# Performance work log

Measured on AMD Instinct MI355X. Metric: run time of the kernel, lower is better.

The kernel has to match this reference:

```python
import jax, jax.numpy as jnp
import numpy as np

N_EXPERTS = 64
TOPK = 4
DIM = 2048
B_T = 8192


def setup_inputs() -> dict:
    key = jax.random.key(0)
    k1, k2 = jax.random.split(key)
    x = jax.random.normal(k1, (B_T, DIM), jnp.float32)
    W = jax.random.normal(k2, (N_EXPERTS, DIM), jnp.float32) * 0.02  # nn.Linear weight (out, in)
    router_bias = jnp.zeros((N_EXPERTS,), jnp.float32)  # registered buffer, init zeros
    return {"x": x, "W": W, "router_bias": router_bias, "token_capacity": 3072}


def _route(x, W, router_bias, token_capacity):
    """Faithful serial greedy capacity-aware routing.

    Replicates the torch nested loop (k-major, token-minor order):
      - per step, pick argmax over the token's (mutated) logits among experts
        with remaining capacity;
      - full experts whose logit exceeds the chosen one get permanently set
        to -inf in that token's logit row (exactly what the inner while-style
        loop does);
      - if no expert has capacity, selected stays -1, weight 0, and the whole
        row becomes -inf (torch sets the top expert to -inf n_experts times).
    """
    logits0 = x @ W.T + router_bias                       # (N, E)
    scores = jax.nn.softmax(logits0, axis=-1)             # (N, E)
    cap = token_capacity // TOPK                          # python int
    remaining0 = jnp.full((N_EXPERTS,), float(cap), jnp.float32)
    N = x.shape[0]
    NEG = jnp.float32(-jnp.inf)

    def step(carry, i):
        logits, remaining = carry
        b = i % N                                         # token index (k-major order)
        row = logits[b]                                   # (E,)
        masked = jnp.where(remaining > 0, row, NEG)
        chosen = jnp.argmax(masked)
        ok = remaining[chosen] > 0                        # False only if all experts full
        sel = jnp.where(ok, chosen, -1).astype(jnp.int32)
        w = jnp.where(ok, scores[b, chosen], jnp.float32(0.0))
        full = remaining <= 0
        cval = row[chosen]
        # full experts 'above' the chosen one were visited and zapped to -inf
        new_row = jnp.where(ok,
                            jnp.where(full & (row > cval), NEG, row),
                            jnp.full_like(row, NEG))
        logits = logits.at[b].set(new_row)
        remaining = remaining.at[chosen].add(jnp.where(ok, jnp.float32(-1.0), jnp.float32(0.0)))
        return (logits, remaining), (sel, w)

    (_, _), (sel_f, w_f) = jax.lax.scan(step, (logits0, remaining0),
                                        jnp.arange(TOPK * N))
    selected = sel_f.reshape(TOPK, N).T                   # (N, TOPK)
    weights = w_f.reshape(TOPK, N).T                      # (N, TOPK)
    weights = weights / (weights.sum(axis=-1, keepdims=True) + 1e-8)
    return selected, weights


def reference(x, W, router_bias, token_capacity):
    return _route(x, W, router_bias, token_capacity)
```

## Files before the change

### kernel.cpp

```cpp
#include <hip/hip_runtime.h>
#include <math.h>

#define N_TOK 8192
#define DIM   2048
#define NE    64
#define TOPK  4
#define THETA 2e-3f
#define TPB   32
#define NBLK  (N_TOK / TPB)
#define HSTR  16

typedef short bf16x8 __attribute__((ext_vector_type(8)));
typedef float f32x4  __attribute__((ext_vector_type(4)));

#define OFF_LOGITS 0
#define OFF_MAXV   (OFF_LOGITS + N_TOK * NE)
#define OFF_DENOM  (OFF_MAXV + N_TOK)
#define OFF_HIST   (OFF_DENOM + N_TOK)
#define OFF_WT     (OFF_HIST + NE * HSTR)
#define OFF_WTMP   (OFF_WT + NE * DIM)

__device__ inline void cvt2(float a, float b, unsigned& hi, unsigned& lo) {
    const unsigned ua = __float_as_uint(a), ub = __float_as_uint(b);
    hi = __builtin_amdgcn_perm(ub, ua, 0x07060302u);
    const float ra = a - __uint_as_float(ua & 0xFFFF0000u);
    const float rb = b - __uint_as_float(ub & 0xFFFF0000u);
    lo = __builtin_amdgcn_perm(__float_as_uint(rb), __float_as_uint(ra), 0x07060302u);
}

union FragU { unsigned u[4]; bf16x8 v; uint4 q; };

__device__ inline void make_frags(const float4& p, const float4& q,
                                  bf16x8& hi, bf16x8& lo) {
    FragU H, L;
    cvt2(p.x, p.y, H.u[0], L.u[0]);
    cvt2(p.z, p.w, H.u[1], L.u[1]);
    cvt2(q.x, q.y, H.u[2], L.u[2]);
    cvt2(q.z, q.w, H.u[3], L.u[3]);
    hi = H.v; lo = L.v;
}

__global__ __launch_bounds__(256)
void k_wc(const float* __restrict__ W, float* __restrict__ wt,
          int* __restrict__ hist) {
    const int t = blockIdx.x * 256 + threadIdx.x;
    if (t < NE * HSTR) hist[t] = 0;
    const int l  = t & 63;
    const int grp = t >> 6;
    const int nt = grp & 3;
    const int kc = grp >> 2;
    const int e  = nt * 16 + (l & 15);
    const int k0 = kc * 32 + (l >> 4) * 8;

    const float4 p = *reinterpret_cast<const float4*>(W + (size_t)e * DIM + k0);
    const float4 q = *reinterpret_cast<const float4*>(W + (size_t)e * DIM + k0 + 4);
    wt[(size_t)(k0 + 0) * NE + e] = p.x;
    wt[(size_t)(k0 + 1) * NE + e] = p.y;
    wt[(size_t)(k0 + 2) * NE + e] = p.z;
    wt[(size_t)(k0 + 3) * NE + e] = p.w;
    wt[(size_t)(k0 + 4) * NE + e] = q.x;
    wt[(size_t)(k0 + 5) * NE + e] = q.y;
    wt[(size_t)(k0 + 6) * NE + e] = q.z;
    wt[(size_t)(k0 + 7) * NE + e] = q.w;
}

__global__ __launch_bounds__(512, 2)
void k_main(const float* __restrict__ x, const float* __restrict__ W,
            const float* __restrict__ bias, const float* __restrict__ wt,
            float* __restrict__ logits, float* __restrict__ maxv,
            float* __restrict__ denomv, int* __restrict__ hist,
            float* __restrict__ out) {
    __shared__ float red[8][TPB][68];
    __shared__ float lbuf[TPB][68];
    __shared__ int   selS[TPB];
    __shared__ float wS[TPB];
    __shared__ short flagIdx[TPB];
    __shared__ int   flagCnt;

    const int tid = threadIdx.x;
    const int w   = tid >> 6;
    const int l   = tid & 63;
    const int t0  = blockIdx.x * TPB;
    const int m   = l & 15;
    const int g   = l >> 4;

    if (tid == 0) flagCnt = 0;

    const float* aP0 = x + (size_t)(t0 + m) * DIM + w * 32 + g * 8;
    const float* aP1 = aP0 + (size_t)16 * DIM;
    const float* bP  = W + (size_t)m * DIM + w * 32 + g * 8;

    f32x4 accA[2][4], accB[2][4];
    #pragma unroll
    for (int t = 0; t < 2; ++t)
        #pragma unroll
        for (int nt = 0; nt < 4; ++nt)
            #pragma unroll
            for (int r = 0; r < 4; ++r) { accA[t][nt][r] = 0.0f; accB[t][nt][r] = 0.0f; }

    float4 cA[2][4], cB[2][8];
    cA[0][0] = *reinterpret_cast<const float4*>(aP0);
    cA[0][1] = *reinterpret_cast<const float4*>(aP0 + 4);
    cA[0][2] = *reinterpret_cast<const float4*>(aP1);
    cA[0][3] = *reinterpret_cast<const float4*>(aP1 + 4);
    #pragma unroll
    for (int nt = 0; nt < 4; ++nt) {
        cB[0][nt * 2 + 0] = *reinterpret_cast<const float4*>(bP + (size_t)nt * 16 * DIM);
        cB[0][nt * 2 + 1] = *reinterpret_cast<const float4*>(bP + (size_t)nt * 16 * DIM + 4);
    }

    #pragma unroll
    for (int win = 0; win < 8; ++win) {
        const int cur = win & 1, nxt = cur ^ 1;
        if (win < 7) {
            const int ko = (win + 1) * 256;
            cA[nxt][0] = *reinterpret_cast<const float4*>(aP0 + ko);
            cA[nxt][1] = *reinterpret_cast<const float4*>(aP0 + ko + 4);
            cA[nxt][2] = *reinterpret_cast<const float4*>(aP1 + ko);
            cA[nxt][3] = *reinterpret_cast<const float4*>(aP1 + ko + 4);
            #pragma unroll
            for (int nt = 0; nt < 4; ++nt) {
                cB[nxt][nt * 2 + 0] =
                    *reinterpret_cast<const float4*>(bP + (size_t)nt * 16 * DIM + ko);
                cB[nxt][nt * 2 + 1] =
                    *reinterpret_cast<const float4*>(bP + (size_t)nt * 16 * DIM + ko + 4);
            }
        }

        bf16x8 bh[4], bl[4];
        #pragma unroll
        for (int nt = 0; nt < 4; ++nt)
            make_frags(cB[cur][nt * 2], cB[cur][nt * 2 + 1], bh[nt], bl[nt]);

        #pragma unroll
        for (int t = 0; t < 2; ++t) {
            bf16x8 ah, al;
            make_frags(cA[cur][t * 2], cA[cur][t * 2 + 1], ah, al);
            #pragma unroll
            for (int nt = 0; nt < 4; ++nt) {
                accA[t][nt] = __builtin_amdgcn_mfma_f32_16x16x32_bf16(ah, bh[nt], accA[t][nt], 0, 0, 0);
                accB[t][nt] = __builtin_amdgcn_mfma_f32_16x16x32_bf16(al, bh[nt], accB[t][nt], 0, 0, 0);
            }
            #pragma unroll
            for (int nt = 0; nt < 4; ++nt)
                accB[t][nt] = __builtin_amdgcn_mfma_f32_16x16x32_bf16(ah, bl[nt], accB[t][nt], 0, 0, 0);
        }
    }

    #pragma unroll
    for (int t = 0; t < 2; ++t)
        #pragma unroll
        for (int nt = 0; nt < 4; ++nt)
            #pragma unroll
            for (int r = 0; r < 4; ++r)
                red[w][t * 16 + g * 4 + r][nt * 16 + m] = accA[t][nt][r] + accB[t][nt][r];
    __syncthreads();

    for (int e2 = tid; e2 < TPB * NE; e2 += 512) {
        const int t = e2 >> 6, e = e2 & 63;
        float s = red[0][t][e];
        #pragma unroll
        for (int ww = 1; ww < 8; ++ww) s += red[ww][t][e];
        s += bias[e];
        logits[(size_t)(t0 + t) * NE + e] = s;
        lbuf[t][e] = s;
    }
    __syncthreads();

    #pragma unroll
    for (int tt = 0; tt < 4; ++tt) {
        const int t = w * 4 + tt;
        const float lv = lbuf[t][l];
        float v1 = lv; int i1 = l; float v2 = -INFINITY;
        #pragma unroll
        for (int off = 32; off; off >>= 1) {
            const float ov1 = __shfl_xor(v1, off);
            const int   oi1 = __shfl_xor(i1, off);
            const float ov2 = __shfl_xor(v2, off);
            if (ov1 > v1 || (ov1 == v1 && oi1 < i1)) {
                v2 = fmaxf(v1, ov2); v1 = ov1; i1 = oi1;
            } else {
                v2 = fmaxf(v2, ov1);
            }
        }
        float s = expf(lv - v1);
        #pragma unroll
        for (int off = 32; off; off >>= 1) s += __shfl_xor(s, off);
        if (l == 0) {
            const int row = t0 + t;
            maxv[row]   = v1;
            denomv[row] = s;
            selS[t]     = i1;
            wS[t]       = 1.0f / s;
            if (v1 - v2 < THETA) {
                const int ix = atomicAdd(&flagCnt, 1);
                flagIdx[ix] = (short)t;
            }
        }
    }
    __syncthreads();

    const int nf = flagCnt;
    for (int fi = 0; fi < nf; ++fi) {
        const int tl  = flagIdx[fi];
        const int row = t0 + tl;
        const float* xr = x + (size_t)row * DIM + w * 256;
        const float* wb = wt + (size_t)(w * 256) * NE + l;
        float a0 = 0.0f, a1 = 0.0f;
        #pragma unroll 4
        for (int k = 0; k < 256; k += 8) {
            const float4 x0 = *reinterpret_cast<const float4*>(xr + k);
            const float4 x1 = *reinterpret_cast<const float4*>(xr + k + 4);
            a0 = fmaf(x0.x, wb[(size_t)(k + 0) * NE], a0);
            a0 = fmaf(x0.y, wb[(size_t)(k + 1) * NE], a0);
            a0 = fmaf(x0.z, wb[(size_t)(k + 2) * NE], a0);
            a0 = fmaf(x0.w, wb[(size_t)(k + 3) * NE], a0);
            a1 = fmaf(x1.x, wb[(size_t)(k + 4) * NE], a1);
            a1 = fmaf(x1.y, wb[(size_t)(k + 5) * NE], a1);
            a1 = fmaf(x1.z, wb[(size_t)(k + 6) * NE], a1);
            a1 = fmaf(x1.w, wb[(size_t)(k + 7) * NE], a1);
        }
        red[w][0][l] = a0 + a1;
        __syncthreads();
        if (w == 0) {
            float lg = bias[l];
            #pragma unroll
            for (int s2 = 0; s2 < 8; ++s2) lg += red[s2][0][l];
            logits[(size_t)row * NE + l] = lg;
            float v = lg; int idx = l;
            #pragma unroll
            for (int off = 32; off; off >>= 1) {
                const float ov = __shfl_xor(v, off);
                const int   oi = __shfl_xor(idx, off);
                if (ov > v || (ov == v && oi < idx)) { v = ov; idx = oi; }
            }
            float p = expf(lg - v);
            #pragma unroll
            for (int off = 32; off; off >>= 1) p += __shfl_xor(p, off);
            if (l == 0) {
                maxv[row]   = v;
                denomv[row] = p;
                selS[tl]    = idx;
                wS[tl]      = 1.0f / p;
            }
        }
        __syncthreads();
    }

    if (w == 0) {
        int cnt = 0;
        #pragma unroll
        for (int t = 0; t < TPB; ++t) cnt += (selS[t] == l) ? 1 : 0;
        if (cnt) atomicAdd(&hist[l * HSTR], cnt);
    }

    if (tid < TPB) {
        const int row = t0 + tid;
        const float se = (float)selS[tid];
        const float wv = wS[tid];
        const float wn = wv / (4.0f * wv + 1e-8f);
        *reinterpret_cast<float4*>(out + (size_t)row * 4) = make_float4(se, se, se, se);
        *reinterpret_cast<float4*>(out + (size_t)N_TOK * TOPK + (size_t)row * 4) =
            make_float4(wn, wn, wn, wn);
    }
}

__global__ __launch_bounds__(256)
void k_decide(const int* __restrict__ hist, const float* __restrict__ logits,
              const float* __restrict__ maxv, const float* __restrict__ denomv,
              const int* __restrict__ tc, float* __restrict__ out,
              float* __restrict__ wtmp) {
    __shared__ int flagS;
    const int tid = threadIdx.x;
    const int cap = tc[0] / TOPK;
    if (tid < NE) {
        const bool bad = (TOPK * hist[tid * HSTR] > cap);
        const unsigned long long mm = __ballot(bad);
        if (tid == 0) flagS = (mm == 0ull) ? 1 : 0;
    }
    __syncthreads();
    if (flagS) return;

    if (tid < 64) {
        const int e = tid;
        int rem = cap;
        for (int k = 0; k < TOPK; ++k) {
            for (int b = 0; b < N_TOK; ++b) {
                const float lg = logits[(size_t)b * NE + e];
                float v = (rem > 0) ? lg : -INFINITY;
                int idx = e;
                #pragma unroll
                for (int off = 32; off; off >>= 1) {
                    const float ov = __shfl_xor(v, off);
                    const int   oi = __shfl_xor(idx, off);
                    if (ov > v || (ov == v && oi < idx)) { v = ov; idx = oi; }
                }
                const bool ok = (v != -INFINITY);
                if (ok && e == idx) rem -= 1;
                const float lc = __shfl(lg, idx);
                if (e == 0) {
                    out[(size_t)b * TOPK + k]  = ok ? (float)idx : -1.0f;
                    wtmp[(size_t)b * TOPK + k] = ok ? expf(lc - maxv[b]) / denomv[b] : 0.0f;
                }
            }
        }
    }
    __syncthreads();
    for (int b = tid; b < N_TOK; b += 256) {
        const float w0 = wtmp[b * 4 + 0], w1_ = wtmp[b * 4 + 1];
        const float w2 = wtmp[b * 4 + 2], w3 = wtmp[b * 4 + 3];
        const float s = ((w0 + w1_) + w2) + w3 + 1e-8f;
        out[N_TOK * TOPK + b * 4 + 0] = w0 / s;
        out[N_TOK * TOPK + b * 4 + 1] = w1_ / s;
        out[N_TOK * TOPK + b * 4 + 2] = w2 / s;
        out[N_TOK * TOPK + b * 4 + 3] = w3 / s;
    }
}

extern "C" void kernel_launch(void* const* d_in, const int* in_sizes, int n_in,
                              void* d_out, int out_size, void* d_ws, size_t ws_size,
                              hipStream_t stream) {
    const float* x    = (const float*)d_in[0];
    const float* W    = (const float*)d_in[1];
    const float* bias = (const float*)d_in[2];
    const int*   tc   = (const int*)d_in[3];

    float* ws       = (float*)d_ws;
    float* logits   = ws + OFF_LOGITS;
    float* maxv     = ws + OFF_MAXV;
    float* denomv   = ws + OFF_DENOM;
    int*   hist     = (int*)(ws + OFF_HIST);
    float* wt       = ws + OFF_WT;
    float* wtmp     = ws + OFF_WTMP;
    float* out      = (float*)d_out;

    k_wc<<<NE * DIM / 8 / 256, 256, 0, stream>>>(W, wt, hist);
    k_main<<<NBLK, 512, 0, stream>>>(x, W, bias, wt, logits, maxv, denomv,
                                     hist, out);
    k_decide<<<1, 256, 0, stream>>>(hist, logits, maxv, denomv, tc, out, wtmp);
}
```

Before: 149.2 us.

## Precompute W hi/lo bf16 fragments in fragment order and halve tokens per block

The weight split into bf16 hi/lo parts now happens once in the prep kernel, which stores them in MFMA-fragment order. The main kernel then loads ready-made fragments with vector loads instead of converting W in every block. Tokens per block drop from 32 to 16, doubling the grid, and launch bounds now ask for 4 blocks per CU to raise occupancy. In exchange each block reads W once for fewer tokens, so weight traffic per token roughly doubles, and the explicit double-buffered prefetch is gone.

```diff
diff --git a/kernel.cpp b/kernel.cpp
--- a/kernel.cpp
+++ b/kernel.cpp
@@ -6,7 +6,7 @@
 #define NE    64
 #define TOPK  4
 #define THETA 2e-3f
-#define TPB   32
+#define TPB   16
 #define NBLK  (N_TOK / TPB)
 #define HSTR  16
 
@@ -17,7 +17,9 @@
 #define OFF_MAXV   (OFF_LOGITS + N_TOK * NE)
 #define OFF_DENOM  (OFF_MAXV + N_TOK)
 #define OFF_HIST   (OFF_DENOM + N_TOK)
-#define OFF_WT     (OFF_HIST + NE * HSTR)
+#define OFF_WH     (OFF_HIST + NE * HSTR)
+#define OFF_WL     (OFF_WH + NE * DIM / 2)
+#define OFF_WT     (OFF_WL + NE * DIM / 2)
 #define OFF_WTMP   (OFF_WT + NE * DIM)
 
 __device__ inline void cvt2(float a, float b, unsigned& hi, unsigned& lo) {
@@ -41,7 +43,8 @@
 }
 
 __global__ __launch_bounds__(256)
-void k_wc(const float* __restrict__ W, float* __restrict__ wt,
+void k_wc(const float* __restrict__ W, unsigned short* __restrict__ wh2,
+          unsigned short* __restrict__ wl2, float* __restrict__ wt,
           int* __restrict__ hist) {
     const int t = blockIdx.x * 256 + threadIdx.x;
     if (t < NE * HSTR) hist[t] = 0;
@@ -54,6 +57,15 @@
 
     const float4 p = *reinterpret_cast<const float4*>(W + (size_t)e * DIM + k0);
     const float4 q = *reinterpret_cast<const float4*>(W + (size_t)e * DIM + k0 + 4);
+    FragU H, L;
+    cvt2(p.x, p.y, H.u[0], L.u[0]);
+    cvt2(p.z, p.w, H.u[1], L.u[1]);
+    cvt2(q.x, q.y, H.u[2], L.u[2]);
+    cvt2(q.z, q.w, H.u[3], L.u[3]);
+    const size_t off = (size_t)grp * 512 + l * 8;
+    *reinterpret_cast<uint4*>(wh2 + off) = H.q;
+    *reinterpret_cast<uint4*>(wl2 + off) = L.q;
+
     wt[(size_t)(k0 + 0) * NE + e] = p.x;
     wt[(size_t)(k0 + 1) * NE + e] = p.y;
     wt[(size_t)(k0 + 2) * NE + e] = p.z;
@@ -64,9 +76,10 @@
     wt[(size_t)(k0 + 7) * NE + e] = q.w;
 }
 
-__global__ __launch_bounds__(512, 2)
-void k_main(const float* __restrict__ x, const float* __restrict__ W,
-            const float* __restrict__ bias, const float* __restrict__ wt,
+__global__ __launch_bounds__(512, 4)
+void k_main(const float* __restrict__ x, const unsigned short* __restrict__ wh2,
+            const unsigned short* __restrict__ wl2, const float* __restrict__ bias,
+            const float* __restrict__ wt,
             float* __restrict__ logits, float* __restrict__ maxv,
             float* __restrict__ denomv, int* __restrict__ hist,
             float* __restrict__ out) {
@@ -86,74 +99,50 @@
 
     if (tid == 0) flagCnt = 0;
 
-    const float* aP0 = x + (size_t)(t0 + m) * DIM + w * 32 + g * 8;
-    const float* aP1 = aP0 + (size_t)16 * DIM;
-    const float* bP  = W + (size_t)m * DIM + w * 32 + g * 8;
-
-    f32x4 accA[2][4], accB[2][4];
+    const float* aP = x + (size_t)(t0 + m) * DIM + w * 32 + g * 8;
+    const unsigned short* bh = wh2 + (size_t)w * 2048 + l * 8;
+    const unsigned short* bl = wl2 + (size_t)w * 2048 + l * 8;
+
+    f32x4 accA[4], accB[4];
     #pragma unroll
-    for (int t = 0; t < 2; ++t)
-        #pragma unroll
-        for (int nt = 0; nt < 4; ++nt)
-            #pragma unroll
-            for (int r = 0; r < 4; ++r) { accA[t][nt][r] = 0.0f; accB[t][nt][r] = 0.0f; }
-
-    float4 cA[2][4], cB[2][8];
-    cA[0][0] = *reinterpret_cast<const float4*>(aP0);
-    cA[0][1] = *reinterpret_cast<const float4*>(aP0 + 4);
-    cA[0][2] = *reinterpret_cast<const float4*>(aP1);
-    cA[0][3] = *reinterpret_cast<const float4*>(aP1 + 4);
-    #pragma unroll
-    for (int nt = 0; nt < 4; ++nt) {
-        cB[0][nt * 2 + 0] = *reinterpret_cast<const float4*>(bP + (size_t)nt * 16 * DIM);
-        cB[0][nt * 2 + 1] = *reinterpret_cast<const float4*>(bP + (size_t)nt * 16 * DIM + 4);
-    }
+    for (int nt = 0; nt < 4; ++nt)
+        #pragma unroll
+        for (int r = 0; r < 4; ++r) { accA[nt][r] = 0.0f; accB[nt][r] = 0.0f; }
 
     #pragma unroll
     for (int win = 0; win < 8; ++win) {
-        const int cur = win & 1, nxt = cur ^ 1;
-        if (win < 7) {
-            const int ko = (win + 1) * 256;
-            cA[nxt][0] = *reinterpret_cast<const float4*>(aP0 + ko);
-            cA[nxt][1] = *reinterpret_cast<const float4*>(aP0 + ko + 4);
-            cA[nxt][2] = *reinterpret_cast<const float4*>(aP1 + ko);
-            cA[nxt][3] = *reinterpret_cast<const float4*>(aP1 + ko + 4);
-            #pragma unroll
-            for (int nt = 0; nt < 4; ++nt) {
-                cB[nxt][nt * 2 + 0] =
-                    *reinterpret_cast<const float4*>(bP + (size_t)nt * 16 * DIM + ko);
-                cB[nxt][nt * 2 + 1] =
-                    *reinterpret_cast<const float4*>(bP + (size_t)nt * 16 * DIM + ko + 4);
-            }
-        }
-
-        bf16x8 bh[4], bl[4];
-        #pragma unroll
-        for (int nt = 0; nt < 4; ++nt)
-            make_frags(cB[cur][nt * 2], cB[cur][nt * 2 + 1], bh[nt], bl[nt]);
-
-        #pragma unroll
-        for (int t = 0; t < 2; ++t) {
-            bf16x8 ah, al;
-            make_frags(cA[cur][t * 2], cA[cur][t * 2 + 1], ah, al);
-            #pragma unroll
-            for (int nt = 0; nt < 4; ++nt) {
-                accA[t][nt] = __builtin_amdgcn_mfma_f32_16x16x32_bf16(ah, bh[nt], accA[t][nt], 0, 0, 0);
-                accB[t][nt] = __builtin_amdgcn_mfma_f32_16x16x32_bf16(al, bh[nt], accB[t][nt], 0, 0, 0);
-            }
-            #pragma unroll
-            for (int nt = 0; nt < 4; ++nt)
-                accB[t][nt] = __builtin_amdgcn_mfma_f32_16x16x32_bf16(ah, bl[nt], accB[t][nt], 0, 0, 0);
+        const float4 p = *reinterpret_cast<const float4*>(aP + win * 256);
+        const float4 q = *reinterpret_cast<const float4*>(aP + win * 256 + 4);
+        uint4 BH[4], BL[4];
+        #pragma unroll
+        for (int nt = 0; nt < 4; ++nt) {
+            BH[nt] = *reinterpret_cast<const uint4*>(
+                bh + (size_t)win * 16384 + nt * 512);
+            BL[nt] = *reinterpret_cast<const uint4*>(
+                bl + (size_t)win * 16384 + nt * 512);
+        }
+
+        bf16x8 ah, al;
+        make_frags(p, q, ah, al);
+
+        #pragma unroll
+        for (int nt = 0; nt < 4; ++nt) {
+            FragU b; b.q = BH[nt];
+            accA[nt] = __builtin_amdgcn_mfma_f32_16x16x32_bf16(ah, b.v, accA[nt], 0, 0, 0);
+            accB[nt] = __builtin_amdgcn_mfma_f32_16x16x32_bf16(al, b.v, accB[nt], 0, 0, 0);
+        }
+        #pragma unroll
+        for (int nt = 0; nt < 4; ++nt) {
+            FragU b; b.q = BL[nt];
+            accB[nt] = __builtin_amdgcn_mfma_f32_16x16x32_bf16(ah, b.v, accB[nt], 0, 0, 0);
         }
     }
 
     #pragma unroll
-    for (int t = 0; t < 2; ++t)
-        #pragma unroll
-        for (int nt = 0; nt < 4; ++nt)
-            #pragma unroll
-            for (int r = 0; r < 4; ++r)
-                red[w][t * 16 + g * 4 + r][nt * 16 + m] = accA[t][nt][r] + accB[t][nt][r];
+    for (int nt = 0; nt < 4; ++nt)
+        #pragma unroll
+        for (int r = 0; r < 4; ++r)
+            red[w][g * 4 + r][nt * 16 + m] = accA[nt][r] + accB[nt][r];
     __syncthreads();
 
     for (int e2 = tid; e2 < TPB * NE; e2 += 512) {
@@ -168,8 +157,8 @@
     __syncthreads();
 
     #pragma unroll
-    for (int tt = 0; tt < 4; ++tt) {
-        const int t = w * 4 + tt;
+    for (int tt = 0; tt < 2; ++tt) {
+        const int t = w * 2 + tt;
         const float lv = lbuf[t][l];
         float v1 = lv; int i1 = l; float v2 = -INFINITY;
         #pragma unroll
@@ -330,12 +319,14 @@
     float* maxv     = ws + OFF_MAXV;
     float* denomv   = ws + OFF_DENOM;
     int*   hist     = (int*)(ws + OFF_HIST);
+    unsigned short* wh2 = (unsigned short*)(ws + OFF_WH);
+    unsigned short* wl2 = (unsigned short*)(ws + OFF_WL);
     float* wt       = ws + OFF_WT;
     float* wtmp     = ws + OFF_WTMP;
     float* out      = (float*)d_out;
 
-    k_wc<<<NE * DIM / 8 / 256, 256, 0, stream>>>(W, wt, hist);
-    k_main<<<NBLK, 512, 0, stream>>>(x, W, bias, wt, logits, maxv, denomv,
-                                     hist, out);
+    k_wc<<<NE * DIM / 8 / 256, 256, 0, stream>>>(W, wh2, wl2, wt, hist);
+    k_main<<<NBLK, 512, 0, stream>>>(x, wh2, wl2, bias, wt, logits, maxv,
+                                     denomv, hist, out);
     k_decide<<<1, 256, 0, stream>>>(hist, logits, maxv, denomv, tc, out, wtmp);
 }
```

After: 131.0 us. 1.14x faster.
